# Performance work log

Measured on AMD Instinct MI355X. Metric: run time of the kernel, lower is better.

## Reference

```python
import jax, jax.numpy as jnp
import numpy as np

N = 50000
E = 800000
IN_C, HID_C, OUT_C = 128, 128, 64


def setup_inputs() -> dict:
    key = jax.random.key(0)
    ks = jax.random.split(key, 12)
    x = jax.random.normal(ks[0], (N, IN_C), dtype=jnp.float32)
    edge_index = jax.random.randint(ks[1], (2, E), 0, N, dtype=jnp.int64)
    dims = [(IN_C, HID_C), (HID_C, HID_C), (HID_C, OUT_C)]
    params = {}
    for i, (din, dout) in enumerate(dims):
        s = 1.0 / np.sqrt(din)
        params[f"Wl{i}"] = jax.random.uniform(ks[2 + 3 * i], (din, dout), jnp.float32, -s, s)
        params[f"b{i}"] = jnp.zeros((dout,), jnp.float32)
        params[f"Wr{i}"] = jax.random.uniform(ks[3 + 3 * i], (din, dout), jnp.float32, -s, s)
    return {"x": x, "edge_index": edge_index, **params}


def _sage_conv(x, src, dst, Wl, b, Wr):
    # mean-aggregate neighbor features: messages flow src -> dst
    agg = jax.ops.segment_sum(x[src], dst, num_segments=N)          # [N, d]
    deg = jax.ops.segment_sum(jnp.ones((src.shape[0],), x.dtype), dst, num_segments=N)
    agg = agg / jnp.maximum(deg, 1.0)[:, None]                      # mean (0 for isolated nodes)
    return agg @ Wl + b + x @ Wr


def reference(x, edge_index, Wl0, b0, Wr0, Wl1, b1, Wr1, Wl2, b2, Wr2):
    src, dst = edge_index[0], edge_index[1]
    h = _sage_conv(x, src, dst, Wl0, b0, Wr0)
    h = jax.nn.relu(h)  # dropout is identity in eval mode
    h = _sage_conv(h, src, dst, Wl1, b1, Wr1)
    h = jax.nn.relu(h)
    h = _sage_conv(h, src, dst, Wl2, b2, Wr2)
    return h
```

## Files before the change

kernel.cpp:

```cpp
#include <hip/hip_runtime.h>

#define N_NODES 50000
#define N_EDGES 800000
#define NBUCK 196
#define NHIST 196

typedef __attribute__((ext_vector_type(8))) short short8;
typedef __attribute__((ext_vector_type(4))) float f32x4;
typedef __attribute__((ext_vector_type(4))) unsigned short ushort4v;
typedef __attribute__((ext_vector_type(8))) unsigned short ushort8v;


__device__ inline void split_bf16(float f, unsigned short& hi, unsigned short& lo) {
    union { float f; unsigned u; } a; a.f = f;
    unsigned r = (a.u + 0x7fffu + ((a.u >> 16) & 1u)) >> 16;
    hi = (unsigned short)r;
    union { unsigned u; float f; } b; b.u = r << 16;
    union { float f; unsigned u; } c; c.f = f - b.f;
    unsigned r2 = (c.u + 0x7fffu + ((c.u >> 16) & 1u)) >> 16;
    lo = (unsigned short)r2;
}

__device__ inline unsigned short f2bf(float f) {
    union { float f; unsigned u; } a; a.f = f;
    return (unsigned short)((a.u + 0x7fffu + ((a.u >> 16) & 1u)) >> 16);
}

__device__ inline float bf2f(unsigned short u) {
    union { unsigned u; float f; } a; a.u = (unsigned)u << 16; return a.f;
}


__global__ void prep_kernel(const float* __restrict__ W0, const float* __restrict__ W1,
                            const float* __restrict__ W2, const float* __restrict__ W3,
                            const float* __restrict__ W4, const float* __restrict__ W5,
                            unsigned short* __restrict__ wout,
                            const float* __restrict__ x, unsigned short* __restrict__ xhi,
                            unsigned short* __restrict__ xlo,
                            const int* __restrict__ dst, int* __restrict__ blkhist) {
    __shared__ int lhist[NBUCK];
    if (blockIdx.x < 320) {
        int t = blockIdx.x * 256 + threadIdx.x;
        const float* W; int D, local, half; size_t base;
        if (t < 65536) {
            int mat = t >> 14; local = t & 16383; D = 128; half = 16384;
            base = (size_t)mat * 32768;
            W = mat == 0 ? W0 : mat == 1 ? W1 : mat == 2 ? W2 : W3;
        } else {
            int m = (t - 65536) >> 13; local = (t - 65536) & 8191; D = 64; half = 8192;
            base = 131072 + (size_t)m * 16384;
            W = m == 0 ? W4 : W5;
        }
        int j = local & 7, lane = (local >> 3) & 63, ks = (local >> 9) & 3, ct = local >> 11;
        int k = ks * 32 + ((lane >> 4) << 3) + j;
        int n = (ct << 4) + (lane & 15);
        unsigned short hi, lo;
        split_bf16(W[k * D + n], hi, lo);
        wout[base + local] = hi;
        wout[base + half + local] = lo;
    } else if (blockIdx.x < 1883) {
        int t = (blockIdx.x - 320) * 256 + threadIdx.x;
        if (t >= N_NODES * 8) return;
        const float* p = x + (size_t)t * 16;
#pragma unroll
        for (int half = 0; half < 2; ++half) {
            float4 v0 = *(const float4*)(p + half * 8);
            float4 v1 = *(const float4*)(p + half * 8 + 4);
            float vv[8] = {v0.x, v0.y, v0.z, v0.w, v1.x, v1.y, v1.z, v1.w};
            ushort8v h, l;
#pragma unroll
            for (int j = 0; j < 8; ++j) {
                unsigned short a, b;
                split_bf16(vv[j], a, b);
                h[j] = a; l[j] = b;
            }
            *(ushort8v*)(xhi + (size_t)t * 16 + half * 8) = h;
            *(ushort8v*)(xlo + (size_t)t * 16 + half * 8) = l;
        }
    } else {
        const int hb = blockIdx.x - 1883;
        const int base = hb * 4096;
        if (threadIdx.x < NBUCK) lhist[threadIdx.x] = 0;
        __syncthreads();
#pragma unroll
        for (int i = 0; i < 16; ++i) {
            int e = base + i * 256 + threadIdx.x;
            if (e < N_EDGES) atomicAdd(&lhist[dst[e] >> 8], 1);
        }
        __syncthreads();
        if (threadIdx.x < NBUCK) blkhist[hb * NBUCK + threadIdx.x] = lhist[threadIdx.x];
    }
}


__global__ void scan_sums_kernel(const int* __restrict__ blkhist,
                                 int* __restrict__ bucketBase, int* __restrict__ bucketCur,
                                 int* __restrict__ rowptr) {
    __shared__ int s[256];
    int tid = threadIdx.x;
    int v = 0;
    if (tid < NBUCK)
        for (int h = 0; h < NHIST; ++h) v += blkhist[h * NBUCK + tid];
    s[tid] = v;
    __syncthreads();
    for (int off = 1; off < 256; off <<= 1) {
        int t = (tid >= off) ? s[tid - off] : 0;
        __syncthreads();
        s[tid] += t;
        __syncthreads();
    }
    if (tid < NBUCK) {
        int b = s[tid] - v;
        bucketBase[tid] = b;
        bucketCur[tid] = b;
    }
    if (tid == 0) { bucketBase[NBUCK] = N_EDGES; rowptr[N_NODES] = N_EDGES; }
}


__global__ __launch_bounds__(256) void partition_kernel(
    const int* __restrict__ src, const int* __restrict__ dst,
    int* __restrict__ bucketCur, unsigned int* __restrict__ ebuf, int E) {
    __shared__ int hist[NBUCK], binoff[NBUCK], bincur[NBUCK], runstart[NBUCK];
    __shared__ int scanbuf[256];
    __shared__ unsigned int sortbuf[2048];
    const int tid = threadIdx.x;
    const int base = blockIdx.x * 2048;
    if (tid < NBUCK) hist[tid] = 0;
    __syncthreads();
    int myb[8]; unsigned int myp[8];
#pragma unroll
    for (int i = 0; i < 8; ++i) {
        int e = base + i * 256 + tid;
        if (e < E) {
            int d = dst[e], s = src[e];
            myb[i] = d >> 8;
            myp[i] = ((unsigned)d << 16) | (unsigned)s;
            atomicAdd(&hist[myb[i]], 1);
        } else myb[i] = -1;
    }
    __syncthreads();
    int v = (tid < NBUCK) ? hist[tid] : 0;
    scanbuf[tid] = v;
    __syncthreads();
    for (int off = 1; off < 256; off <<= 1) {
        int t = (tid >= off) ? scanbuf[tid - off] : 0;
        __syncthreads();
        scanbuf[tid] += t;
        __syncthreads();
    }
    if (tid < NBUCK) {
        binoff[tid] = scanbuf[tid] - v;
        bincur[tid] = 0;
        runstart[tid] = atomicAdd(&bucketCur[tid], v);
    }
    __syncthreads();
#pragma unroll
    for (int i = 0; i < 8; ++i) {
        if (myb[i] >= 0) {
            int r = atomicAdd(&bincur[myb[i]], 1);
            sortbuf[binoff[myb[i]] + r] = myp[i];
        }
    }
    __syncthreads();
    int nloc = E - base; if (nloc > 2048) nloc = 2048;
#pragma unroll
    for (int i = 0; i < 8; ++i) {
        int idx = i * 256 + tid;
        if (idx < nloc) {
            unsigned int p = sortbuf[idx];
            int b = p >> 24;
            ebuf[runstart[b] + (idx - binoff[b])] = p;
        }
    }
}


__global__ __launch_bounds__(256) void fine_fill_kernel(
    const unsigned int* __restrict__ ebuf, const int* __restrict__ bucketBase,
    int* __restrict__ rowptr, unsigned short* __restrict__ esrc, int n) {
    __shared__ int cnt[256], scanbuf[256], cur[256];
    const int b = blockIdx.x, tid = threadIdx.x;
    const int nbase = b << 8;
    cnt[tid] = 0;
    __syncthreads();
    const int lo = bucketBase[b], hi = bucketBase[b + 1];
    for (int k = lo + tid; k < hi; k += 256)
        atomicAdd(&cnt[(ebuf[k] >> 16) & 255], 1);
    __syncthreads();
    int v = cnt[tid];
    scanbuf[tid] = v;
    __syncthreads();
    for (int off = 1; off < 256; off <<= 1) {
        int t = (tid >= off) ? scanbuf[tid - off] : 0;
        __syncthreads();
        scanbuf[tid] += t;
        __syncthreads();
    }
    int start = lo + scanbuf[tid] - v;
    if (nbase + tid < n) rowptr[nbase + tid] = start;
    cur[tid] = start;
    __syncthreads();
    for (int k = lo + tid; k < hi; k += 256) {
        unsigned int p = ebuf[k];
        int pos = atomicAdd(&cur[(p >> 16) & 255], 1);
        esrc[pos] = (unsigned short)(p & 0xFFFFu);
    }
}


template <int DOUT, bool RELU, bool SPLIT_OUT>
__global__ __launch_bounds__(256, 4) void sage_layer(
    const unsigned short* __restrict__ Hhi, const unsigned short* __restrict__ Hlo,
    const int* __restrict__ rowptr, const unsigned short* __restrict__ esrc,
    const unsigned short* __restrict__ B1p, const unsigned short* __restrict__ B2p,
    const float* __restrict__ bias, float* __restrict__ outf,
    unsigned short* __restrict__ outhi, unsigned short* __restrict__ outlo, int M) {
    constexpr int K = 128, BM = 32, KS = 4, CT = DOUT / 16, CPW = CT / 4;
    constexpr int PITCH = K + 8;
    constexpr int HALF = CT * KS * 512;
    __shared__ unsigned short As[3][BM * PITCH];

    const int tid = threadIdx.x;
    const int r0 = blockIdx.x * BM;

    const unsigned short* __restrict__ srcs[2] = {Hhi, Hlo};
#pragma unroll
    for (int s = 0; s < 2; ++s) {
#pragma unroll
        for (int c = 0; c < 2; ++c) {
            int chunk = tid + c * 256;
            int row = chunk >> 4;
            int c8 = (chunk & 15) * 8;
            int grow = r0 + row; if (grow >= M) grow = M - 1;
            *(ushort8v*)(&As[s + 1][row * PITCH + c8]) =
                *(const ushort8v*)(srcs[s] + (size_t)grow * K + c8);
        }
    }

    {
        const int g16 = tid >> 4, l16 = tid & 15;
        for (int nn = 0; nn < 2; ++nn) {
            int row = g16 * 2 + nn;
            int node = r0 + row; if (node >= M) node = M - 1;
            int beg = rowptr[node], end = rowptr[node + 1];
            float a0[8] = {0,0,0,0,0,0,0,0}, a1[8] = {0,0,0,0,0,0,0,0};
            float a2[8] = {0,0,0,0,0,0,0,0}, a3[8] = {0,0,0,0,0,0,0,0};
            int k = beg;
            for (; k + 4 <= end; k += 4) {
                int e0 = esrc[k], e1 = esrc[k + 1], e2 = esrc[k + 2], e3 = esrc[k + 3];
                ushort8v v0 = *(const ushort8v*)(Hhi + (size_t)e0 * 128 + l16 * 8);
                ushort8v v1 = *(const ushort8v*)(Hhi + (size_t)e1 * 128 + l16 * 8);
                ushort8v v2 = *(const ushort8v*)(Hhi + (size_t)e2 * 128 + l16 * 8);
                ushort8v v3 = *(const ushort8v*)(Hhi + (size_t)e3 * 128 + l16 * 8);
#pragma unroll
                for (int j = 0; j < 8; ++j) {
                    a0[j] += bf2f(v0[j]); a1[j] += bf2f(v1[j]);
                    a2[j] += bf2f(v2[j]); a3[j] += bf2f(v3[j]);
                }
            }
            for (; k < end; ++k) {
                int e0 = esrc[k];
                ushort8v v0 = *(const ushort8v*)(Hhi + (size_t)e0 * 128 + l16 * 8);
#pragma unroll
                for (int j = 0; j < 8; ++j) a0[j] += bf2f(v0[j]);
            }
            float inv = (end > beg) ? 1.0f / (float)(end - beg) : 0.0f;
            ushort8v mh;
#pragma unroll
            for (int j = 0; j < 8; ++j)
                mh[j] = f2bf((a0[j] + a1[j] + a2[j] + a3[j]) * inv);
            *(ushort8v*)(&As[0][row * PITCH + l16 * 8]) = mh;
        }
    }
    __syncthreads();

    const int wave = tid >> 6, lane = tid & 63;
    const int rl = lane & 15, quad = lane >> 4;

    f32x4 acc[2][CPW];
#pragma unroll
    for (int c = 0; c < CPW; ++c) {
        float bv = bias[(wave * CPW + c) * 16 + rl];
        acc[0][c] = (f32x4){bv, bv, bv, bv};
        acc[1][c] = acc[0][c];
    }

#pragma unroll
    for (int ks = 0; ks < KS; ++ks) {
        short8 a_ag[2], a_sh[2][2];
#pragma unroll
        for (int rt = 0; rt < 2; ++rt) {
            int off = (rt * 16 + rl) * PITCH + ks * 32 + quad * 8;
            a_ag[rt]    = *(const short8*)(&As[0][off]);
            a_sh[rt][0] = *(const short8*)(&As[1][off]);
            a_sh[rt][1] = *(const short8*)(&As[2][off]);
        }
        short8 b1[CPW][2], b2[CPW][2];
#pragma unroll
        for (int c = 0; c < CPW; ++c) {
            size_t boff = (((wave * CPW + c) * KS + ks) * 64 + lane) * 8;
#pragma unroll
            for (int p = 0; p < 2; ++p) {
                b1[c][p] = *(const short8*)(B1p + p * HALF + boff);
                b2[c][p] = *(const short8*)(B2p + p * HALF + boff);
            }
        }
#pragma unroll
        for (int rt = 0; rt < 2; ++rt)
#pragma unroll
            for (int c = 0; c < CPW; ++c) {
                acc[rt][c] = __builtin_amdgcn_mfma_f32_16x16x32_bf16(a_ag[rt],    b1[c][0], acc[rt][c], 0, 0, 0);
                acc[rt][c] = __builtin_amdgcn_mfma_f32_16x16x32_bf16(a_ag[rt],    b1[c][1], acc[rt][c], 0, 0, 0);
                acc[rt][c] = __builtin_amdgcn_mfma_f32_16x16x32_bf16(a_sh[rt][0], b2[c][0], acc[rt][c], 0, 0, 0);
                acc[rt][c] = __builtin_amdgcn_mfma_f32_16x16x32_bf16(a_sh[rt][0], b2[c][1], acc[rt][c], 0, 0, 0);
                acc[rt][c] = __builtin_amdgcn_mfma_f32_16x16x32_bf16(a_sh[rt][1], b2[c][0], acc[rt][c], 0, 0, 0);
            }
    }

#pragma unroll
    for (int rt = 0; rt < 2; ++rt)
#pragma unroll
        for (int c = 0; c < CPW; ++c) {
            int col = (wave * CPW + c) * 16 + rl;
            int rowb = r0 + rt * 16 + quad * 4;
#pragma unroll
            for (int r = 0; r < 4; ++r) {
                int rr = rowb + r;
                if (rr < M) {
                    float vv = acc[rt][c][r];
                    if (RELU) vv = fmaxf(vv, 0.f);
                    if (SPLIT_OUT) {
                        unsigned short h, l;
                        split_bf16(vv, h, l);
                        outhi[(size_t)rr * DOUT + col] = h;
                        outlo[(size_t)rr * DOUT + col] = l;
                    } else {
                        outf[(size_t)rr * DOUT + col] = vv;
                    }
                }
            }
        }
}


extern "C" void kernel_launch(void* const* d_in, const int* in_sizes, int n_in,
                              void* d_out, int out_size, void* d_ws, size_t ws_size,
                              hipStream_t stream) {
    const float* x   = (const float*)d_in[0];
    const int* eidx  = (const int*)d_in[1];
    const int* src   = eidx;
    const int* dst   = eidx + N_EDGES;
    const float* Wl0 = (const float*)d_in[2];
    const float* b0  = (const float*)d_in[3];
    const float* Wr0 = (const float*)d_in[4];
    const float* Wl1 = (const float*)d_in[5];
    const float* b1  = (const float*)d_in[6];
    const float* Wr1 = (const float*)d_in[7];
    const float* Wl2 = (const float*)d_in[8];
    const float* b2  = (const float*)d_in[9];
    const float* Wr2 = (const float*)d_in[10];
    float* outp = (float*)d_out;

    unsigned short* xhi  = (unsigned short*)d_ws;
    unsigned short* xlo  = xhi + (size_t)N_NODES * 128;
    unsigned short* h1hi = xlo + (size_t)N_NODES * 128;
    unsigned short* h1lo = h1hi + (size_t)N_NODES * 128;
    unsigned int* ebuf = (unsigned int*)h1hi;
    int* rowptr    = (int*)(h1lo + (size_t)N_NODES * 128);
    int* blkhist   = rowptr + 50016;
    int* bucketBase= blkhist + 38416;
    int* bucketCur = bucketBase + 256;
    unsigned short* esrc  = (unsigned short*)(bucketCur + 256);
    unsigned short* packw = esrc + N_EDGES;
    unsigned short* Wl0p = packw;
    unsigned short* Wr0p = packw + 32768;
    unsigned short* Wl1p = packw + 65536;
    unsigned short* Wr1p = packw + 98304;
    unsigned short* Wl2p = packw + 131072;
    unsigned short* Wr2p = packw + 147456;

    prep_kernel<<<2079, 256, 0, stream>>>(Wl0, Wr0, Wl1, Wr1, Wl2, Wr2, packw,
                                          x, xhi, xlo, dst, blkhist);
    scan_sums_kernel<<<1, 256, 0, stream>>>(blkhist, bucketBase, bucketCur, rowptr);
    partition_kernel<<<(N_EDGES + 2047) / 2048, 256, 0, stream>>>(src, dst, bucketCur, ebuf, N_EDGES);
    fine_fill_kernel<<<NBUCK, 256, 0, stream>>>(ebuf, bucketBase, rowptr, esrc, N_NODES);

    const int gemmGrid = (N_NODES + 31) / 32;

    sage_layer<128, true, true><<<gemmGrid, 256, 0, stream>>>(
        xhi, xlo, rowptr, esrc, Wl0p, Wr0p, b0, nullptr, h1hi, h1lo, N_NODES);
    sage_layer<128, true, true><<<gemmGrid, 256, 0, stream>>>(
        h1hi, h1lo, rowptr, esrc, Wl1p, Wr1p, b1, nullptr, xhi, xlo, N_NODES);
    sage_layer<64, false, false><<<gemmGrid, 256, 0, stream>>>(
        xhi, xlo, rowptr, esrc, Wl2p, Wr2p, b2, outp, nullptr, nullptr, N_NODES);
}
```

Baseline: 272.3 us.

## Interleave neighbor gathers for two rows and raise occupancy target

The mean-aggregation phase now walks the neighbor lists of both rows a thread handles in one interleaved loop, issuing eight independent gathered loads per iteration instead of processing the rows one after another. Per-row accumulators drop from four partial arrays to one, which frees registers, and launch bounds are raised from 4 to 6 blocks per CU. The aim is more memory-level parallelism and occupancy to hide latency in this gather-bound phase. The costs are a possible register spill or cap on unrolling from the tighter bound, and a serial add chain in place of four independent accumulators.

```diff
diff --git a/kernel.cpp b/kernel.cpp
--- a/kernel.cpp
+++ b/kernel.cpp
@@ -210,7 +210,7 @@
 
 
 template <int DOUT, bool RELU, bool SPLIT_OUT>
-__global__ __launch_bounds__(256, 4) void sage_layer(
+__global__ __launch_bounds__(256, 6) void sage_layer(
     const unsigned short* __restrict__ Hhi, const unsigned short* __restrict__ Hlo,
     const int* __restrict__ rowptr, const unsigned short* __restrict__ esrc,
     const unsigned short* __restrict__ B1p, const unsigned short* __restrict__ B2p,
@@ -240,38 +240,79 @@
 
     {
         const int g16 = tid >> 4, l16 = tid & 15;
-        for (int nn = 0; nn < 2; ++nn) {
-            int row = g16 * 2 + nn;
-            int node = r0 + row; if (node >= M) node = M - 1;
-            int beg = rowptr[node], end = rowptr[node + 1];
-            float a0[8] = {0,0,0,0,0,0,0,0}, a1[8] = {0,0,0,0,0,0,0,0};
-            float a2[8] = {0,0,0,0,0,0,0,0}, a3[8] = {0,0,0,0,0,0,0,0};
-            int k = beg;
-            for (; k + 4 <= end; k += 4) {
-                int e0 = esrc[k], e1 = esrc[k + 1], e2 = esrc[k + 2], e3 = esrc[k + 3];
-                ushort8v v0 = *(const ushort8v*)(Hhi + (size_t)e0 * 128 + l16 * 8);
-                ushort8v v1 = *(const ushort8v*)(Hhi + (size_t)e1 * 128 + l16 * 8);
-                ushort8v v2 = *(const ushort8v*)(Hhi + (size_t)e2 * 128 + l16 * 8);
-                ushort8v v3 = *(const ushort8v*)(Hhi + (size_t)e3 * 128 + l16 * 8);
-#pragma unroll
-                for (int j = 0; j < 8; ++j) {
-                    a0[j] += bf2f(v0[j]); a1[j] += bf2f(v1[j]);
-                    a2[j] += bf2f(v2[j]); a3[j] += bf2f(v3[j]);
-                }
-            }
-            for (; k < end; ++k) {
-                int e0 = esrc[k];
-                ushort8v v0 = *(const ushort8v*)(Hhi + (size_t)e0 * 128 + l16 * 8);
-#pragma unroll
-                for (int j = 0; j < 8; ++j) a0[j] += bf2f(v0[j]);
-            }
-            float inv = (end > beg) ? 1.0f / (float)(end - beg) : 0.0f;
-            ushort8v mh;
-#pragma unroll
-            for (int j = 0; j < 8; ++j)
-                mh[j] = f2bf((a0[j] + a1[j] + a2[j] + a3[j]) * inv);
-            *(ushort8v*)(&As[0][row * PITCH + l16 * 8]) = mh;
-        }
+        const int rowA = g16 * 2, rowB = rowA + 1;
+        int nodeA = r0 + rowA; if (nodeA >= M) nodeA = M - 1;
+        int nodeB = r0 + rowB; if (nodeB >= M) nodeB = M - 1;
+        const int begA = rowptr[nodeA], endA = rowptr[nodeA + 1];
+        const int begB = rowptr[nodeB], endB = rowptr[nodeB + 1];
+        const unsigned short* __restrict__ Hb = Hhi + l16 * 8;
+        float accA[8] = {0,0,0,0,0,0,0,0}, accB[8] = {0,0,0,0,0,0,0,0};
+        int kA = begA, kB = begB;
+        for (; kA + 4 <= endA && kB + 4 <= endB; kA += 4, kB += 4) {
+            int eA0 = esrc[kA], eA1 = esrc[kA + 1], eA2 = esrc[kA + 2], eA3 = esrc[kA + 3];
+            int eB0 = esrc[kB], eB1 = esrc[kB + 1], eB2 = esrc[kB + 2], eB3 = esrc[kB + 3];
+            ushort8v vA0 = *(const ushort8v*)(Hb + (size_t)eA0 * 128);
+            ushort8v vA1 = *(const ushort8v*)(Hb + (size_t)eA1 * 128);
+            ushort8v vA2 = *(const ushort8v*)(Hb + (size_t)eA2 * 128);
+            ushort8v vA3 = *(const ushort8v*)(Hb + (size_t)eA3 * 128);
+            ushort8v vB0 = *(const ushort8v*)(Hb + (size_t)eB0 * 128);
+            ushort8v vB1 = *(const ushort8v*)(Hb + (size_t)eB1 * 128);
+            ushort8v vB2 = *(const ushort8v*)(Hb + (size_t)eB2 * 128);
+            ushort8v vB3 = *(const ushort8v*)(Hb + (size_t)eB3 * 128);
+#pragma unroll
+            for (int j = 0; j < 8; ++j) {
+                accA[j] += bf2f(vA0[j]); accA[j] += bf2f(vA1[j]);
+                accA[j] += bf2f(vA2[j]); accA[j] += bf2f(vA3[j]);
+                accB[j] += bf2f(vB0[j]); accB[j] += bf2f(vB1[j]);
+                accB[j] += bf2f(vB2[j]); accB[j] += bf2f(vB3[j]);
+            }
+        }
+        for (; kA + 4 <= endA; kA += 4) {
+            int e0 = esrc[kA], e1 = esrc[kA + 1], e2 = esrc[kA + 2], e3 = esrc[kA + 3];
+            ushort8v v0 = *(const ushort8v*)(Hb + (size_t)e0 * 128);
+            ushort8v v1 = *(const ushort8v*)(Hb + (size_t)e1 * 128);
+            ushort8v v2 = *(const ushort8v*)(Hb + (size_t)e2 * 128);
+            ushort8v v3 = *(const ushort8v*)(Hb + (size_t)e3 * 128);
+#pragma unroll
+            for (int j = 0; j < 8; ++j) {
+                accA[j] += bf2f(v0[j]); accA[j] += bf2f(v1[j]);
+                accA[j] += bf2f(v2[j]); accA[j] += bf2f(v3[j]);
+            }
+        }
+        for (; kA < endA; ++kA) {
+            int e0 = esrc[kA];
+            ushort8v v0 = *(const ushort8v*)(Hb + (size_t)e0 * 128);
+#pragma unroll
+            for (int j = 0; j < 8; ++j) accA[j] += bf2f(v0[j]);
+        }
+        for (; kB + 4 <= endB; kB += 4) {
+            int e0 = esrc[kB], e1 = esrc[kB + 1], e2 = esrc[kB + 2], e3 = esrc[kB + 3];
+            ushort8v v0 = *(const ushort8v*)(Hb + (size_t)e0 * 128);
+            ushort8v v1 = *(const ushort8v*)(Hb + (size_t)e1 * 128);
+            ushort8v v2 = *(const ushort8v*)(Hb + (size_t)e2 * 128);
+            ushort8v v3 = *(const ushort8v*)(Hb + (size_t)e3 * 128);
+#pragma unroll
+            for (int j = 0; j < 8; ++j) {
+                accB[j] += bf2f(v0[j]); accB[j] += bf2f(v1[j]);
+                accB[j] += bf2f(v2[j]); accB[j] += bf2f(v3[j]);
+            }
+        }
+        for (; kB < endB; ++kB) {
+            int e0 = esrc[kB];
+            ushort8v v0 = *(const ushort8v*)(Hb + (size_t)e0 * 128);
+#pragma unroll
+            for (int j = 0; j < 8; ++j) accB[j] += bf2f(v0[j]);
+        }
+        float invA = (endA > begA) ? 1.0f / (float)(endA - begA) : 0.0f;
+        float invB = (endB > begB) ? 1.0f / (float)(endB - begB) : 0.0f;
+        ushort8v mA, mB;
+#pragma unroll
+        for (int j = 0; j < 8; ++j) {
+            mA[j] = f2bf(accA[j] * invA);
+            mB[j] = f2bf(accB[j] * invB);
+        }
+        *(ushort8v*)(&As[0][rowA * PITCH + l16 * 8]) = mA;
+        *(ushort8v*)(&As[0][rowB * PITCH + l16 * 8]) = mB;
     }
     __syncthreads();
 
```

Result: no change. 272.8 us (+0.2%).
